# Performance work log

Hardware: AMD Instinct MI355X
Metric: run time of the kernel (lower is better)

The kernel has to match this reference:

```python
import jax, jax.numpy as jnp
import numpy as np

PIXELS_PER_CELL = (8, 8)
CELLS_PER_BLOCK = (2, 2)
ORIENTATIONS = 9
GRAY_W = jnp.array([0.2125, 0.7154, 0.0721], dtype=jnp.float32)  # skimage rgb2gray
EPS = 1e-5  # skimage L2-Hys eps


def setup_inputs() -> dict:
    key = jax.random.key(0)
    x = jax.random.uniform(key, (64, 512, 512, 3), dtype=jnp.float32)
    return {"x": x}


def _hog(x):
    # rgb2gray
    gray = jnp.einsum("bhwc,c->bhw", x, GRAY_W)  # [B,H,W]
    B, H, W = gray.shape
    pr, pc = PIXELS_PER_CELL
    br, bc = CELLS_PER_BLOCK
    O = ORIENTATIONS

    # skimage _hog_channel_gradient: central differences, zero at borders
    g_row = jnp.zeros_like(gray).at[:, 1:-1, :].set(gray[:, 2:, :] - gray[:, :-2, :])
    g_col = jnp.zeros_like(gray).at[:, :, 1:-1].set(gray[:, :, 2:] - gray[:, :, :-2])

    mag = jnp.hypot(g_row, g_col)
    ori = jnp.rad2deg(jnp.arctan2(g_row, g_col)) % 180.0  # unsigned orientation

    ncr, ncc = H // pr, W // pc
    mag = mag[:, : ncr * pr, : ncc * pc]
    ori = ori[:, : ncr * pr, : ncc * pc]

    spacing = 180.0 / O
    cell_area = float(pr * pc)
    # per-orientation-bin cell histograms: hard binning (skimage cell_hog)
    hists = []
    for o in range(O):
        lo, hi = spacing * o, spacing * (o + 1)
        contrib = jnp.where((ori >= lo) & (ori < hi), mag, 0.0)
        # sum over each pr x pc cell, divide by cell area
        h = contrib.reshape(B, ncr, pr, ncc, pc).sum(axis=(2, 4)) / cell_area
        hists.append(h)
    hist = jnp.stack(hists, axis=-1)  # [B, ncr, ncc, O]

    # overlapping blocks of cells, stride 1 cell
    nbr, nbc = ncr - br + 1, ncc - bc + 1
    block = jnp.stack(
        [jnp.stack([hist[:, r : r + nbr, c : c + nbc, :] for c in range(bc)], axis=3)
         for r in range(br)], axis=3)  # [B, nbr, nbc, br, bc, O]

    # L2-Hys normalization (skimage default block_norm)
    norm = jnp.sqrt(jnp.sum(block * block, axis=(3, 4, 5), keepdims=True) + EPS ** 2)
    blk = jnp.minimum(block / norm, 0.2)
    norm2 = jnp.sqrt(jnp.sum(blk * blk, axis=(3, 4, 5), keepdims=True) + EPS ** 2)
    blk = blk / norm2

    return blk.reshape(B, -1).astype(jnp.float32)


def reference(x):
    return _hog(x)
```

## Files before the change

### kernel.cpp

```cpp
#include <hip/hip_runtime.h>
#include <math.h>

#define IMG_H 512
#define IMG_W 512
#define NCELL 64
#define NORI 9

__device__ __forceinline__ float fdlibm_atanf_inl(float x) {
#pragma clang fp contract(off)
    const float one = 1.0f;
    int hx = __float_as_int(x);
    int ix = hx & 0x7fffffff;
    int id;
    if (ix >= 0x4c800000) {
        const float v = 1.5707962513e+00f + 7.5497894159e-08f;
        return (hx > 0) ? v : -v;
    }
    if (ix < 0x3ee00000) {
        if (ix < 0x39800000) return x;
        id = -1;
    } else {
        x = fabsf(x);
        if (ix < 0x3f980000) {
            if (ix < 0x3f300000) { id = 0; x = (2.0f * x - one) / (2.0f + x); }
            else                 { id = 1; x = (x - one) / (x + one); }
        } else {
            if (ix < 0x401c0000) { id = 2; x = (x - 1.5f) / (one + 1.5f * x); }
            else                 { id = 3; x = -1.0f / x; }
        }
    }
    float z = x * x;
    float w = z * z;
    float s1 = z * (3.3333334327e-01f + w * (1.4285714924e-01f + w * (9.0908870101e-02f
             + w * (6.6610731184e-02f + w * (4.9768779427e-02f + w * 1.6285819933e-02f)))));
    float s2 = w * (-2.0000000298e-01f + w * (-1.1111110449e-01f + w * (-7.6918758452e-02f
             + w * (-5.8335702866e-02f + w * -3.6531571299e-02f))));
    if (id < 0) return x - x * (s1 + s2);
    const float hi = (id == 0) ? 4.6364760399e-01f : (id == 1) ? 7.8539812565e-01f
                   : (id == 2) ? 9.8279368877e-01f : 1.5707962513e+00f;
    const float lo = (id == 0) ? 5.0121582440e-09f : (id == 1) ? 3.7748947079e-08f
                   : (id == 2) ? 3.4473217170e-08f : 7.5497894159e-08f;
    z = hi - ((x * (s1 + s2) - lo) - x);
    return (hx < 0) ? -z : z;
}

__device__ __forceinline__ int fdlibm_bin_inl(float y, float x) {
#pragma clang fp contract(off)
    const float tiny   = 1.0e-30f;
    const float pi_o_2 = 1.5707963705e+00f;
    const float pi     = 3.1415927410e+00f;
    const float pi_lo  = -8.7422776573e-08f;

    int hx = __float_as_int(x), ix = hx & 0x7fffffff;
    int hy = __float_as_int(y), iy = hy & 0x7fffffff;
    float th;
    if (hx == 0x3f800000) { th = fdlibm_atanf_inl(y); }
    else {
        int m = ((hy >> 31) & 1) | ((hx >> 30) & 2);
        if (iy == 0) {
            switch (m) {
                case 0:
                case 1: th = y; break;
                case 2: th =  pi + tiny; break;
                default: th = -pi - tiny; break;
            }
        } else if (ix == 0) {
            th = (hy < 0) ? -pi_o_2 - tiny : pi_o_2 + tiny;
        } else {
            int k = (iy - ix) >> 23;
            float z;
            int mm = m;
            if (k > 26) {
                z = pi_o_2 + 0.5f * pi_lo;
                mm &= 1;
            } else if (k < -26 && hx < 0) {
                z = 0.0f;
            } else {
                z = fdlibm_atanf_inl(fabsf(y / x));
            }
            switch (mm) {
                case 0:  th = z; break;
                case 1:  th = -z; break;
                case 2:  th = pi - (z - pi_lo); break;
                default: th = (z - pi_lo) - pi; break;
            }
        }
    }
    const float RAD2DEG = (float)(180.0 / 3.14159265358979311600e+00);
    float m = fmodf(th * RAD2DEG, 180.0f);
    if (m < 0.0f) m += 180.0f;
    int o = (int)(m * 0.05f);
    if (o < 9) {
        if (m < 20.0f * (float)o) --o;
        else if (m >= 20.0f * (float)(o + 1)) ++o;
    }
    return o;
}

__global__ __launch_bounds__(512, 4) void hog_fused_kernel(const float* __restrict__ x,
                                                           float* __restrict__ out) {
#pragma clang fp contract(off)
    const int bid = blockIdx.x;
    const int b   = bid >> 3;
    const int s   = bid & 7;
    const int r0  = s * 8;
    const int SL  = (s == 7) ? 7 : 8;
    const int t   = threadIdx.x;

    __shared__ __align__(16) float gbuf[3][8][IMG_W];
    __shared__ __align__(16) float histL[2][NCELL * NORI];

    const float GW0 = 0.2125f, GW1 = 0.7154f, GW2 = 0.0721f;
    const float PIF   = 3.14159265358979323846f;
    const float PIO2F = 1.57079632679489662f;
    const float PIO4F = 0.78539816339744831f;

    {
        float4 A[6], C[6], D[6];
#pragma unroll
        for (int k = 0; k < 6; ++k) {
            const int gi = k >> 1;
            const int pq = t + 512 * (k & 1);
            const int rr = pq >> 7, grp = pq & 127;
            int h = (r0 - 1 + gi) * 8 + rr;
            if (h < 0)   h = 1;
            if (h > 511) h = 510;
            const float4* p4 = (const float4*)x + (size_t)(b * IMG_H + h) * (IMG_W * 3 / 4)
                               + (size_t)grp * 3;
            A[k] = p4[0]; C[k] = p4[1]; D[k] = p4[2];
        }
#pragma unroll
        for (int k = 0; k < 6; ++k) {
            const int gi = k >> 1;
            const int sl = (r0 - 1 + gi + 3) % 3;
            const int pq = t + 512 * (k & 1);
            const int rr = pq >> 7, wg = (pq & 127) * 4;
            float4 gv;
            gv.x = __builtin_fmaf(A[k].z, GW2, __builtin_fmaf(A[k].y, GW1, A[k].x * GW0));
            gv.y = __builtin_fmaf(C[k].y, GW2, __builtin_fmaf(C[k].x, GW1, A[k].w * GW0));
            gv.z = __builtin_fmaf(D[k].x, GW2, __builtin_fmaf(C[k].w, GW1, C[k].z * GW0));
            gv.w = __builtin_fmaf(D[k].w, GW2, __builtin_fmaf(D[k].z, GW1, D[k].y * GW0));
            *(float4*)&gbuf[sl][rr][wg] = gv;
        }
    }
    __syncthreads();

    const int w   = t;
    const int wl  = (w == 0)   ? 0   : w - 1;
    const int wr  = (w == 511) ? 511 : w + 1;
    const bool wok = (w >= 1) && (w <= 510);
    const int c   = w >> 3;
    const int jl  = t & 7;

    for (int r = r0; r <= r0 + SL; ++r) {
        const bool pf = (r < r0 + SL);
        float4 A[2], C[2], D[2];
        if (pf) {
#pragma unroll
            for (int k = 0; k < 2; ++k) {
                const int pq = t + 512 * k;
                const int rr = pq >> 7, grp = pq & 127;
                int h = (r + 2) * 8 + rr;
                if (h > 511) h = 510;
                const float4* p4 = (const float4*)x + (size_t)(b * IMG_H + h) * (IMG_W * 3 / 4)
                                   + (size_t)grp * 3;
                A[k] = p4[0]; C[k] = p4[1]; D[k] = p4[2];
            }
        }

        const int slA = (r + 2) % 3;
        const int slB = r % 3;
        const int slC = (r + 1) % 3;
        float cc[10], ee[8], ww[8];
        cc[0] = gbuf[slA][7][w];
        cc[9] = gbuf[slC][0][w];
#pragma unroll
        for (int i = 0; i < 8; ++i) {
            cc[i + 1] = gbuf[slB][i][w];
            ee[i]     = gbuf[slB][i][wr];
            ww[i]     = gbuf[slB][i][wl];
        }

        float bh[9];
#pragma unroll
        for (int k = 0; k < 9; ++k) bh[k] = 0.0f;

#pragma unroll
        for (int j = 0; j < 8; ++j) {
            const float gr = cc[j + 2] - cc[j];
            const float gc = wok ? (ee[j] - ww[j]) : 0.0f;
            const float mag = __builtin_amdgcn_sqrtf(__builtin_fmaf(gr, gr, gc * gc));

            const float ax = fabsf(gc), ay = fabsf(gr);
            const float mx = fmaxf(ax, ay), mn = fminf(ax, ay);
            const bool red = mn > 0.4142135624f * mx;
            const float num = red ? (mn - mx) : mn;
            const float den = red ? (mn + mx) : mx;
            const float xx  = num * __builtin_amdgcn_rcpf(den);
            const float z   = xx * xx;
            float y = __builtin_fmaf(
                        __builtin_fmaf(
                          __builtin_fmaf(8.05374449538e-2f, z, -1.38776856032e-1f),
                          z, 1.99777106478e-1f),
                        z, -3.33329491539e-1f);
            float r0a = __builtin_fmaf(y * z, xx, xx);
            if (red)        r0a = PIO4F + r0a;
            if (ay > ax)    r0a = PIO2F - r0a;
            if (gc < 0.0f)  r0a = PIF - r0a;
            if (gr < 0.0f)  r0a = PIF - r0a;
            const float q    = (r0a * 57.295779513082323f) * 0.05f;
            int o            = (int)q;
            const float frac = q - (float)o;
            bool suspect = (frac < 1e-4f) || (frac > 0.9999f) || (o > 8);
            if (ay == 0.0f) { o = 0; suspect = false; }
            if (__builtin_expect(suspect, 0)) {
                o = fdlibm_bin_inl(gr, gc);
            }
#pragma unroll
            for (int k = 0; k < 9; ++k) bh[k] += (o == k) ? mag : 0.0f;
        }

#pragma unroll
        for (int k = 0; k < 9; ++k) {
            bh[k] += __shfl_xor(bh[k], 1, 64);
            bh[k] += __shfl_xor(bh[k], 2, 64);
            bh[k] += __shfl_xor(bh[k], 4, 64);
        }
        float mv = bh[0];
#pragma unroll
        for (int k = 1; k < 8; ++k) mv = (jl == k) ? bh[k] : mv;
        histL[r & 1][c * NORI + jl] = mv * 0.015625f;
        if (jl == 0) histL[r & 1][c * NORI + 8] = bh[8] * 0.015625f;

        __syncthreads();

        if (pf) {
#pragma unroll
            for (int k = 0; k < 2; ++k) {
                const int pq = t + 512 * k;
                const int rr = pq >> 7, wg = (pq & 127) * 4;
                float4 gv;
                gv.x = __builtin_fmaf(A[k].z, GW2, __builtin_fmaf(A[k].y, GW1, A[k].x * GW0));
                gv.y = __builtin_fmaf(C[k].y, GW2, __builtin_fmaf(C[k].x, GW1, A[k].w * GW0));
                gv.z = __builtin_fmaf(D[k].x, GW2, __builtin_fmaf(C[k].w, GW1, C[k].z * GW0));
                gv.w = __builtin_fmaf(D[k].w, GW2, __builtin_fmaf(D[k].z, GW1, D[k].y * GW0));
                *(float4*)&gbuf[slA][rr][wg] = gv;
            }
        }

        if (r > r0 && t < 252) {
            const int cb = t >> 2;
            const int l  = t & 3;
            const int bi = l >> 1, bj = l & 1;
            const int br = r - 1;
            const float* v = &histL[(br + bi) & 1][(cb + bj) * NORI];
            float vv[9];
            float ss = 0.0f;
#pragma unroll
            for (int k = 0; k < 9; ++k) { vv[k] = v[k]; ss += vv[k] * vv[k]; }
            ss += __shfl_xor(ss, 1, 64);
            ss += __shfl_xor(ss, 2, 64);
            const float rn1 = 1.0f / sqrtf(ss + 1e-10f);
            float ss2 = 0.0f;
#pragma unroll
            for (int k = 0; k < 9; ++k) { vv[k] = fminf(vv[k] * rn1, 0.2f); ss2 += vv[k] * vv[k]; }
            ss2 += __shfl_xor(ss2, 1, 64);
            ss2 += __shfl_xor(ss2, 2, 64);
            const float rn2 = 1.0f / sqrtf(ss2 + 1e-10f);
            float* od = out + (size_t)(b * 63 + br) * (63 * 36) + (cb * 36 + l * 9);
#pragma unroll
            for (int k = 0; k < 9; ++k) od[k] = vv[k] * rn2;
        }

        __syncthreads();
    }
}

extern "C" void kernel_launch(void* const* d_in, const int* in_sizes, int n_in,
                              void* d_out, int out_size, void* d_ws, size_t ws_size,
                              hipStream_t stream) {
    const float* x = (const float*)d_in[0];
    float* out     = (float*)d_out;
    (void)d_ws; (void)ws_size;

    hog_fused_kernel<<<dim3(64 * 8), dim3(512), 0, stream>>>(x, out);
}
```

Before: 307.8 us.

## Split fused HOG into per-cell-row histogram kernel and separate normalization kernel

```diff
diff --git a/kernel.cpp b/kernel.cpp
--- a/kernel.cpp
+++ b/kernel.cpp
@@ -97,50 +97,45 @@
     return o;
 }
 
-__global__ __launch_bounds__(512, 4) void hog_fused_kernel(const float* __restrict__ x,
-                                                           float* __restrict__ out) {
+__global__ __launch_bounds__(512, 6) void hog_hist_kernel(const float* __restrict__ x,
+                                                          float* __restrict__ hist) {
 #pragma clang fp contract(off)
     const int bid = blockIdx.x;
-    const int b   = bid >> 3;
-    const int s   = bid & 7;
-    const int r0  = s * 8;
-    const int SL  = (s == 7) ? 7 : 8;
+    const int b   = bid >> 6;
+    const int cr  = bid & 63;
     const int t   = threadIdx.x;
-
-    __shared__ __align__(16) float gbuf[3][8][IMG_W];
-    __shared__ __align__(16) float histL[2][NCELL * NORI];
+    const int h0  = cr * 8;
+
+    __shared__ __align__(16) float g[10][IMG_W];
 
     const float GW0 = 0.2125f, GW1 = 0.7154f, GW2 = 0.0721f;
-    const float PIF   = 3.14159265358979323846f;
-    const float PIO2F = 1.57079632679489662f;
-    const float PIO4F = 0.78539816339744831f;
-
-    {
-        float4 A[6], C[6], D[6];
-#pragma unroll
-        for (int k = 0; k < 6; ++k) {
-            const int gi = k >> 1;
-            const int pq = t + 512 * (k & 1);
-            const int rr = pq >> 7, grp = pq & 127;
-            int h = (r0 - 1 + gi) * 8 + rr;
+    float4 A[3], C[3], D[3];
+#pragma unroll
+    for (int k = 0; k < 3; ++k) {
+        const int gi = t + 512 * k;
+        if (k < 2 || t < 256) {
+            const int rr = gi >> 7;
+            int h = h0 - 1 + rr;
             if (h < 0)   h = 1;
             if (h > 511) h = 510;
+            const int grp = gi & 127;
             const float4* p4 = (const float4*)x + (size_t)(b * IMG_H + h) * (IMG_W * 3 / 4)
                                + (size_t)grp * 3;
             A[k] = p4[0]; C[k] = p4[1]; D[k] = p4[2];
         }
-#pragma unroll
-        for (int k = 0; k < 6; ++k) {
-            const int gi = k >> 1;
-            const int sl = (r0 - 1 + gi + 3) % 3;
-            const int pq = t + 512 * (k & 1);
-            const int rr = pq >> 7, wg = (pq & 127) * 4;
+    }
+#pragma unroll
+    for (int k = 0; k < 3; ++k) {
+        const int gi = t + 512 * k;
+        if (k < 2 || t < 256) {
+            const int rr = gi >> 7;
+            const int wg = (gi & 127) * 4;
             float4 gv;
             gv.x = __builtin_fmaf(A[k].z, GW2, __builtin_fmaf(A[k].y, GW1, A[k].x * GW0));
             gv.y = __builtin_fmaf(C[k].y, GW2, __builtin_fmaf(C[k].x, GW1, A[k].w * GW0));
             gv.z = __builtin_fmaf(D[k].x, GW2, __builtin_fmaf(C[k].w, GW1, C[k].z * GW0));
             gv.w = __builtin_fmaf(D[k].w, GW2, __builtin_fmaf(D[k].z, GW1, D[k].y * GW0));
-            *(float4*)&gbuf[sl][rr][wg] = gv;
+            *(float4*)&g[rr][wg] = gv;
         }
     }
     __syncthreads();
@@ -152,128 +147,92 @@
     const int c   = w >> 3;
     const int jl  = t & 7;
 
-    for (int r = r0; r <= r0 + SL; ++r) {
-        const bool pf = (r < r0 + SL);
-        float4 A[2], C[2], D[2];
-        if (pf) {
-#pragma unroll
-            for (int k = 0; k < 2; ++k) {
-                const int pq = t + 512 * k;
-                const int rr = pq >> 7, grp = pq & 127;
-                int h = (r + 2) * 8 + rr;
-                if (h > 511) h = 510;
-                const float4* p4 = (const float4*)x + (size_t)(b * IMG_H + h) * (IMG_W * 3 / 4)
-                                   + (size_t)grp * 3;
-                A[k] = p4[0]; C[k] = p4[1]; D[k] = p4[2];
-            }
-        }
-
-        const int slA = (r + 2) % 3;
-        const int slB = r % 3;
-        const int slC = (r + 1) % 3;
-        float cc[10], ee[8], ww[8];
-        cc[0] = gbuf[slA][7][w];
-        cc[9] = gbuf[slC][0][w];
-#pragma unroll
-        for (int i = 0; i < 8; ++i) {
-            cc[i + 1] = gbuf[slB][i][w];
-            ee[i]     = gbuf[slB][i][wr];
-            ww[i]     = gbuf[slB][i][wl];
-        }
-
-        float bh[9];
-#pragma unroll
-        for (int k = 0; k < 9; ++k) bh[k] = 0.0f;
-
-#pragma unroll
-        for (int j = 0; j < 8; ++j) {
-            const float gr = cc[j + 2] - cc[j];
-            const float gc = wok ? (ee[j] - ww[j]) : 0.0f;
-            const float mag = __builtin_amdgcn_sqrtf(__builtin_fmaf(gr, gr, gc * gc));
-
-            const float ax = fabsf(gc), ay = fabsf(gr);
-            const float mx = fmaxf(ax, ay), mn = fminf(ax, ay);
-            const bool red = mn > 0.4142135624f * mx;
-            const float num = red ? (mn - mx) : mn;
-            const float den = red ? (mn + mx) : mx;
-            const float xx  = num * __builtin_amdgcn_rcpf(den);
-            const float z   = xx * xx;
-            float y = __builtin_fmaf(
-                        __builtin_fmaf(
-                          __builtin_fmaf(8.05374449538e-2f, z, -1.38776856032e-1f),
-                          z, 1.99777106478e-1f),
-                        z, -3.33329491539e-1f);
-            float r0a = __builtin_fmaf(y * z, xx, xx);
-            if (red)        r0a = PIO4F + r0a;
-            if (ay > ax)    r0a = PIO2F - r0a;
-            if (gc < 0.0f)  r0a = PIF - r0a;
-            if (gr < 0.0f)  r0a = PIF - r0a;
-            const float q    = (r0a * 57.295779513082323f) * 0.05f;
-            int o            = (int)q;
-            const float frac = q - (float)o;
-            bool suspect = (frac < 1e-4f) || (frac > 0.9999f) || (o > 8);
-            if (ay == 0.0f) { o = 0; suspect = false; }
-            if (__builtin_expect(suspect, 0)) {
-                o = fdlibm_bin_inl(gr, gc);
-            }
-#pragma unroll
-            for (int k = 0; k < 9; ++k) bh[k] += (o == k) ? mag : 0.0f;
-        }
-
-#pragma unroll
-        for (int k = 0; k < 9; ++k) {
-            bh[k] += __shfl_xor(bh[k], 1, 64);
-            bh[k] += __shfl_xor(bh[k], 2, 64);
-            bh[k] += __shfl_xor(bh[k], 4, 64);
-        }
-        float mv = bh[0];
-#pragma unroll
-        for (int k = 1; k < 8; ++k) mv = (jl == k) ? bh[k] : mv;
-        histL[r & 1][c * NORI + jl] = mv * 0.015625f;
-        if (jl == 0) histL[r & 1][c * NORI + 8] = bh[8] * 0.015625f;
-
-        __syncthreads();
-
-        if (pf) {
-#pragma unroll
-            for (int k = 0; k < 2; ++k) {
-                const int pq = t + 512 * k;
-                const int rr = pq >> 7, wg = (pq & 127) * 4;
-                float4 gv;
-                gv.x = __builtin_fmaf(A[k].z, GW2, __builtin_fmaf(A[k].y, GW1, A[k].x * GW0));
-                gv.y = __builtin_fmaf(C[k].y, GW2, __builtin_fmaf(C[k].x, GW1, A[k].w * GW0));
-                gv.z = __builtin_fmaf(D[k].x, GW2, __builtin_fmaf(C[k].w, GW1, C[k].z * GW0));
-                gv.w = __builtin_fmaf(D[k].w, GW2, __builtin_fmaf(D[k].z, GW1, D[k].y * GW0));
-                *(float4*)&gbuf[slA][rr][wg] = gv;
-            }
-        }
-
-        if (r > r0 && t < 252) {
-            const int cb = t >> 2;
-            const int l  = t & 3;
-            const int bi = l >> 1, bj = l & 1;
-            const int br = r - 1;
-            const float* v = &histL[(br + bi) & 1][(cb + bj) * NORI];
-            float vv[9];
-            float ss = 0.0f;
-#pragma unroll
-            for (int k = 0; k < 9; ++k) { vv[k] = v[k]; ss += vv[k] * vv[k]; }
-            ss += __shfl_xor(ss, 1, 64);
-            ss += __shfl_xor(ss, 2, 64);
-            const float rn1 = 1.0f / sqrtf(ss + 1e-10f);
-            float ss2 = 0.0f;
-#pragma unroll
-            for (int k = 0; k < 9; ++k) { vv[k] = fminf(vv[k] * rn1, 0.2f); ss2 += vv[k] * vv[k]; }
-            ss2 += __shfl_xor(ss2, 1, 64);
-            ss2 += __shfl_xor(ss2, 2, 64);
-            const float rn2 = 1.0f / sqrtf(ss2 + 1e-10f);
-            float* od = out + (size_t)(b * 63 + br) * (63 * 36) + (cb * 36 + l * 9);
-#pragma unroll
-            for (int k = 0; k < 9; ++k) od[k] = vv[k] * rn2;
-        }
-
-        __syncthreads();
-    }
+    float cc[10], ee[8], ww[8];
+#pragma unroll
+    for (int i = 0; i < 10; ++i) cc[i] = g[i][w];
+#pragma unroll
+    for (int i = 0; i < 8; ++i) { ee[i] = g[i + 1][wr]; ww[i] = g[i + 1][wl]; }
+
+    const float CK[8] = { 0.9396926208f,  0.7660444431f,  0.5f,            0.1736481777f,
+                         -0.1736481777f, -0.5f,           -0.7660444431f, -0.9396926208f };
+    const float SK[8] = { 0.3420201433f,  0.6427876097f,  0.8660254038f,  0.9848077530f,
+                          0.9848077530f,  0.8660254038f,  0.6427876097f,  0.3420201433f };
+
+    float bh[9];
+#pragma unroll
+    for (int k = 0; k < 9; ++k) bh[k] = 0.0f;
+
+#pragma unroll
+    for (int r = 0; r < 8; ++r) {
+        const float gr = cc[r + 2] - cc[r];
+        const float gc = wok ? (ee[r] - ww[r]) : 0.0f;
+        const float mag = __builtin_amdgcn_sqrtf(__builtin_fmaf(gr, gr, gc * gc));
+
+        const float gy = fabsf(gr);
+        const float gx = (gr < 0.0f) ? -gc : gc;
+        const float th = 1e-4f * mag;
+        int  o = 0;
+        bool suspect = false;
+#pragma unroll
+        for (int k = 0; k < 8; ++k) {
+            const float ck = __builtin_fmaf(gy, CK[k], -(gx * SK[k]));
+            o += (ck >= 0.0f) ? 1 : 0;
+            suspect = suspect || (fabsf(ck) < th);
+        }
+        suspect = suspect || ((gx < 0.0f) && (gy < 1e-5f * fabsf(gc)));
+        if (gy == 0.0f) { o = 0; suspect = false; }
+        if (__builtin_expect(suspect, 0)) {
+            o = fdlibm_bin_inl(gr, gc);
+        }
+#pragma unroll
+        for (int k = 0; k < 9; ++k) bh[k] += (o == k) ? mag : 0.0f;
+    }
+
+#pragma unroll
+    for (int k = 0; k < 9; ++k) {
+        bh[k] += __shfl_xor(bh[k], 1, 64);
+        bh[k] += __shfl_xor(bh[k], 2, 64);
+        bh[k] += __shfl_xor(bh[k], 4, 64);
+    }
+    float mv = bh[0];
+#pragma unroll
+    for (int k = 1; k < 8; ++k) mv = (jl == k) ? bh[k] : mv;
+    float* hout = hist + (size_t)(b * NCELL + cr) * (NCELL * NORI);
+    hout[c * NORI + jl] = mv * 0.015625f;
+    if (jl == 0) hout[c * NORI + 8] = bh[8] * 0.015625f;
+}
+
+__global__ __launch_bounds__(256) void hog_norm_kernel(const float* __restrict__ hist,
+                                                       float* __restrict__ out) {
+#pragma clang fp contract(off)
+    const int bid = blockIdx.x;
+    const int b   = bid / 63;
+    const int r   = bid % 63;
+    const int t   = threadIdx.x;
+    const int c   = t >> 2;
+    const int l   = t & 3;
+    if (c >= 63) return;
+
+    const int bi = l >> 1, bj = l & 1;
+    const float* v = hist + ((size_t)(b * NCELL + r + bi) * NCELL + (c + bj)) * NORI;
+
+    float vv[9];
+    float ss = 0.0f;
+#pragma unroll
+    for (int k = 0; k < 9; ++k) { vv[k] = v[k]; ss += vv[k] * vv[k]; }
+    ss += __shfl_xor(ss, 1, 64);
+    ss += __shfl_xor(ss, 2, 64);
+    const float rn1 = 1.0f / sqrtf(ss + 1e-10f);
+    float ss2 = 0.0f;
+#pragma unroll
+    for (int k = 0; k < 9; ++k) { vv[k] = fminf(vv[k] * rn1, 0.2f); ss2 += vv[k] * vv[k]; }
+    ss2 += __shfl_xor(ss2, 1, 64);
+    ss2 += __shfl_xor(ss2, 2, 64);
+    const float rn2 = 1.0f / sqrtf(ss2 + 1e-10f);
+
+    float* od = out + (size_t)bid * (63 * 36) + (c * 36 + l * 9);
+#pragma unroll
+    for (int k = 0; k < 9; ++k) od[k] = vv[k] * rn2;
 }
 
 extern "C" void kernel_launch(void* const* d_in, const int* in_sizes, int n_in,
@@ -281,7 +240,8 @@
                               hipStream_t stream) {
     const float* x = (const float*)d_in[0];
     float* out     = (float*)d_out;
-    (void)d_ws; (void)ws_size;
-
-    hog_fused_kernel<<<dim3(64 * 8), dim3(512), 0, stream>>>(x, out);
-}
+    float* hist    = (float*)d_ws;
+
+    hog_hist_kernel<<<dim3(64 * 64), dim3(512), 0, stream>>>(x, hist);
+    hog_norm_kernel<<<dim3(64 * 63), dim3(256), 0, stream>>>(hist, out);
+}
```

Result: faster. 296.8 us (-3.6%).
